# Kernel optimization log

Measured on AMD Instinct MI355X. Metric: run time of the kernel, lower is better.

The kernel has to match this reference:

```python
import jax, jax.numpy as jnp
import numpy as np
from jax import lax

EPS = 1e-5

def _instance_norm(x):
    # per-sample, per-channel over HW, affine=False (torch default), biased var
    m = jnp.mean(x, axis=(2, 3), keepdims=True)
    v = jnp.mean((x - m) ** 2, axis=(2, 3), keepdims=True)
    return (x - m) / jnp.sqrt(v + EPS)

def _lrelu(x):
    return jax.nn.leaky_relu(x, 0.2)

def _conv(x, w, b, stride=1, pad=0):
    y = lax.conv_general_dilated(x, w, (stride, stride), ((pad, pad), (pad, pad)),
                                 dimension_numbers=('NCHW', 'OIHW', 'NCHW'))
    return y + b[None, :, None, None]

def _conv_transpose(x, w, b):
    # torch ConvTranspose2d(k=3, stride=2, padding=1, output_padding=1)
    # == dilated conv with lhs_dilation=2, pad (k-1-p, k-1-p+op) = (1, 2),
    # kernel spatially flipped and in/out swapped. w: (Cin, Cout, 3, 3)
    wt = jnp.flip(w, axis=(2, 3)).transpose(1, 0, 2, 3)  # (Cout, Cin, 3, 3)
    y = lax.conv_general_dilated(x, wt, (1, 1), ((1, 2), (1, 2)),
                                 lhs_dilation=(2, 2),
                                 dimension_numbers=('NCHW', 'OIHW', 'NCHW'))
    return y + b[None, :, None, None]

def _reflect_pad1(x):
    return jnp.pad(x, ((0, 0), (0, 0), (1, 1), (1, 1)), mode='reflect')

def _nearest_resize(x, out_h, out_w):
    in_h, in_w = x.shape[2], x.shape[3]
    iy = (jnp.arange(out_h) * (in_h / out_h)).astype(jnp.int32)
    ix = (jnp.arange(out_w) * (in_w / out_w)).astype(jnp.int32)
    return x[:, :, iy][:, :, :, ix]

def setup_inputs() -> dict:
    key = jax.random.key(0)
    ks = jax.random.split(key, 12)
    B, S, H, W = 8, 19, 256, 256
    out_nc = 512
    inp = jax.random.normal(ks[0], (B, 3, H, W), dtype=jnp.float32)
    labels = jax.random.randint(ks[1], (B, 1, H, W), 0, S)
    segmap = (labels == jnp.arange(S).reshape(1, S, 1, 1)).astype(jnp.float32)
    sc = 0.05
    return {
        'input': inp, 'segmap': segmap,
        'w1': jax.random.normal(ks[2], (32, 3, 3, 3), jnp.float32) * sc,
        'b1': jnp.zeros((32,), jnp.float32),
        'w2': jax.random.normal(ks[3], (64, 32, 3, 3), jnp.float32) * sc,
        'b2': jnp.zeros((64,), jnp.float32),
        'w3': jax.random.normal(ks[4], (128, 64, 3, 3), jnp.float32) * sc,
        'b3': jnp.zeros((128,), jnp.float32),
        'w4': jax.random.normal(ks[5], (128, 256, 3, 3), jnp.float32) * sc,  # torch convT layout (Cin, Cout, kh, kw)
        'b4': jnp.zeros((256,), jnp.float32),
        'w5': jax.random.normal(ks[6], (out_nc, 256, 3, 3), jnp.float32) * sc,
        'b5': jnp.zeros((out_nc,), jnp.float32),
    }

def _backbone(x, w1, b1, w2, b2, w3, b3, w4, b4, w5, b5):
    x = _lrelu(_instance_norm(_conv(_reflect_pad1(x), w1, b1)))          # [B,32,256,256]
    x = _lrelu(_instance_norm(_conv(x, w2, b2, stride=2, pad=1)))        # [B,64,128,128]
    x = _lrelu(_instance_norm(_conv(x, w3, b3, stride=2, pad=1)))        # [B,128,64,64]
    x = _lrelu(_instance_norm(_conv_transpose(x, w4, b4)))               # [B,256,128,128]
    x = jnp.tanh(_conv(_reflect_pad1(x), w5, b5))                        # [B,512,128,128]
    return x

def reference(input, segmap, w1, b1, w2, b2, w3, b3, w4, b4, w5, b5):
    codes = _backbone(input, w1, b1, w2, b2, w3, b3, w4, b4, w5, b5)
    seg = _nearest_resize(segmap, codes.shape[2], codes.shape[3])
    mask = (seg > 0).astype(codes.dtype)                                  # segmap.bool()
    sums = jnp.einsum('bchw,bshw->bsc', codes, mask)                      # masked sum per (b, class)
    counts = jnp.sum(mask, axis=(2, 3))[:, :, None]                       # [B,S,1]
    return jnp.where(counts > 0, sums / jnp.maximum(counts, 1.0), 0.0)    # [B,S,C]
```

## Files before the change

kernel.cpp:

```cpp
#include <hip/hip_runtime.h>

#define LB __launch_bounds__(256)

constexpr int S = 19;

typedef __attribute__((ext_vector_type(8))) short frag16;
typedef __attribute__((ext_vector_type(8))) ushort ushort8;
typedef __attribute__((ext_vector_type(4))) float f32x4;

__device__ __forceinline__ int reflect256(int i) { return i < 0 ? -i : (i > 255 ? 510 - i : i); }
__device__ __forceinline__ int reflect128(int i) { return i < 0 ? -i : (i > 127 ? 254 - i : i); }

__device__ __forceinline__ ushort f2bf(float f) {
    union { float f; uint u; } a; a.f = f;
    uint r = a.u + 0x7fffu + ((a.u >> 16) & 1u);
    return (ushort)(r >> 16);
}
__device__ __forceinline__ float bf2f(ushort u) {
    union { uint u; float f; } a; a.u = ((uint)u) << 16; return a.f;
}

__device__ __forceinline__ void gll16(const void* g, void* l) {
    __builtin_amdgcn_global_load_lds(
        (const __attribute__((address_space(1))) void*)g,
        (__attribute__((address_space(3))) void*)l, 16, 0, 0);
}

__global__ LB void k_conv1cl(const float* __restrict__ in, const float* __restrict__ w,
                             const float* __restrict__ bias, ushort* __restrict__ out) {
    __shared__ float Wr[864];
    __shared__ float Bs[32];
    int t = threadIdx.x;
    for (int e = t; e < 864; e += 256) Wr[e] = w[e];
    if (t < 32) Bs[t] = bias[t];
    __syncthreads();
    int idx = blockIdx.x * 256 + t;
    int x = idx & 255, y = (idx >> 8) & 255, b = idx >> 16;
    float v[27];
    #pragma unroll
    for (int ci = 0; ci < 3; ++ci) {
        const float* ip = in + ((b * 3 + ci) << 16);
        #pragma unroll
        for (int ky = 0; ky < 3; ++ky) {
            int iy = reflect256(y + ky - 1);
            #pragma unroll
            for (int kx = 0; kx < 3; ++kx) {
                int ix = reflect256(x + kx - 1);
                v[ci * 9 + ky * 3 + kx] = ip[(iy << 8) + ix];
            }
        }
    }
    ushort* op = out + (long)idx * 32;
    #pragma unroll
    for (int g = 0; g < 4; ++g) {
        ushort8 o;
        #pragma unroll
        for (int j = 0; j < 8; ++j) {
            int co = g * 8 + j;
            float a = Bs[co];
            #pragma unroll
            for (int k = 0; k < 27; ++k) a += v[k] * Wr[co * 27 + k];
            o[j] = f2bf(a);
        }
        *(ushort8*)(op + g * 8) = o;
    }
}

template <int C, int PB, int SPLITS>
__global__ LB void k_stats_cl(const ushort* __restrict__ x,
                              float* __restrict__ psum, float* __restrict__ pss) {
    __shared__ float lsum[C], lss[C];
    int b = blockIdx.x / SPLITS, sp = blockIdx.x % SPLITS;
    int t = threadIdx.x;
    if (t < C) { lsum[t] = 0.f; lss[t] = 0.f; }
    __syncthreads();
    constexpr int CG = C / 8;
    constexpr int PO = 256 / CG;
    int c0 = (t % CG) * 8;
    int po = t / CG;
    float s[8], ss[8];
    #pragma unroll
    for (int k = 0; k < 8; ++k) { s[k] = 0.f; ss[k] = 0.f; }
    const ushort* base = x + ((long)b * SPLITS + sp) * (long)PB * C;
    for (int p = po; p < PB; p += PO) {
        ushort8 v = *(const ushort8*)(base + (long)p * C + c0);
        #pragma unroll
        for (int k = 0; k < 8; ++k) {
            float f = bf2f(v[k]);
            s[k] += f; ss[k] += f * f;
        }
    }
    #pragma unroll
    for (int k = 0; k < 8; ++k) {
        atomicAdd(&lsum[c0 + k], s[k]);
        atomicAdd(&lss[c0 + k], ss[k]);
    }
    __syncthreads();
    if (t < C) {
        psum[blockIdx.x * C + t] = lsum[t];
        pss[blockIdx.x * C + t] = lss[t];
    }
}

template <int C, int SPLITS, int P>
__global__ LB void k_red_cl(const float* __restrict__ psum, const float* __restrict__ pss,
                            float* __restrict__ mean, float* __restrict__ istd) {
    int idx = blockIdx.x * 256 + threadIdx.x;
    if (idx >= 8 * C) return;
    int b = idx / C, c = idx % C;
    float s = 0.f, ss = 0.f;
    for (int sp = 0; sp < SPLITS; ++sp) {
        s += psum[(b * SPLITS + sp) * C + c];
        ss += pss[(b * SPLITS + sp) * C + c];
    }
    float m = s / (float)P;
    float v = ss / (float)P - m * m;
    mean[idx] = m;
    istd[idx] = rsqrtf(v + 1e-5f);
}

template <int C, int P>
__global__ LB void k_nl_cl(ushort* __restrict__ x, const float* __restrict__ mean,
                           const float* __restrict__ istd) {
    long e = ((long)blockIdx.x * 256 + threadIdx.x) * 8;
    int c0 = (int)(e % C);
    int b = (int)(e / ((long)P * C));
    ushort8 v = *(ushort8*)(x + e);
    const float* mp = mean + b * C + c0;
    const float* ip = istd + b * C + c0;
    #pragma unroll
    for (int k = 0; k < 8; ++k) {
        float u = (bf2f(v[k]) - mp[k]) * ip[k];
        u = u > 0.f ? u : 0.2f * u;
        v[k] = f2bf(u);
    }
    *(ushort8*)(x + e) = v;
}

__global__ LB void k_wtall(const float* __restrict__ w2, const float* __restrict__ w3,
                           const float* __restrict__ w4, const float* __restrict__ w5,
                           ushort* __restrict__ t2, ushort* __restrict__ t3,
                           ushort* __restrict__ t4, ushort* __restrict__ t5) {
    int e = blockIdx.x * 256 + threadIdx.x;
    if (e < 18432) {
        int ci = e & 31, co = (e >> 5) & 63, tap = e >> 11;
        t2[e] = f2bf(w2[(co * 32 + ci) * 9 + tap]);
    } else if (e < 18432 + 73728) {
        int e2 = e - 18432;
        int ci = e2 & 63, co = (e2 >> 6) & 127, tap = e2 >> 13;
        t3[e2] = f2bf(w3[(co * 64 + ci) * 9 + tap]);
    } else if (e < 18432 + 73728 + 294912) {
        int e3 = e - (18432 + 73728);
        int ci = e3 & 127, co = (e3 >> 7) & 255, tap = e3 >> 15;
        t4[e3] = f2bf(w4[ci * 2304 + co * 9 + tap]);
    } else {
        int e4 = e - (18432 + 73728 + 294912);
        int ci = e4 & 255, co = (e4 >> 8) & 511, tap = e4 >> 17;
        t5[e4] = f2bf(w5[(co * 256 + ci) * 9 + tap]);
    }
}

__global__ LB void k_conv2m(const ushort* __restrict__ xin, const ushort* __restrict__ wt,
                            const float* __restrict__ bias, ushort* __restrict__ xout) {
    int bx = blockIdx.x;
    int y = bx & 127, b = bx >> 7;
    int t = threadIdx.x, w = t >> 6, lane = t & 63;
    int col0 = w * 32;
    int lanep = lane & 15, hi = lane >> 4;

    f32x4 acc[4][2];
    #pragma unroll
    for (int m = 0; m < 4; ++m)
        #pragma unroll
        for (int n = 0; n < 2; ++n) acc[m][n] = (f32x4){0.f, 0.f, 0.f, 0.f};

    #pragma unroll
    for (int ky = 0; ky < 3; ++ky) {
        int iy = 2 * y + ky - 1;
        if (iy < 0) continue;
        #pragma unroll
        for (int kx = 0; kx < 3; ++kx) {
            int tap = ky * 3 + kx;
            const ushort* wb = wt + ((tap * 64 + lanep) << 5) + hi * 8;
            frag16 av[4];
            #pragma unroll
            for (int m = 0; m < 4; ++m) av[m] = *(const frag16*)(wb + ((m * 16) << 5));
            frag16 bv[2];
            #pragma unroll
            for (int n = 0; n < 2; ++n) {
                int xo = col0 + n * 16 + lanep;
                int ix = 2 * xo + kx - 1;
                frag16 vv = (frag16)(short)0;
                if (ix >= 0)
                    vv = *(const frag16*)(xin + ((((long)(b * 256 + iy)) << 8) + ix) * 32 + hi * 8);
                bv[n] = vv;
            }
            #pragma unroll
            for (int m = 0; m < 4; ++m)
                #pragma unroll
                for (int n = 0; n < 2; ++n)
                    acc[m][n] = __builtin_amdgcn_mfma_f32_16x16x32_bf16(av[m], bv[n], acc[m][n], 0, 0, 0);
        }
    }
    float bvv[4][4];
    #pragma unroll
    for (int m = 0; m < 4; ++m)
        #pragma unroll
        for (int r = 0; r < 4; ++r) bvv[m][r] = bias[m * 16 + hi * 4 + r];
    #pragma unroll
    for (int n = 0; n < 2; ++n) {
        int xo = col0 + n * 16 + lanep;
        long pb = ((((long)(b * 128 + y)) << 7) + xo) * 64 + hi * 4;
        #pragma unroll
        for (int m = 0; m < 4; ++m) {
            ushort4 o;
            o.x = f2bf(acc[m][n][0] + bvv[m][0]);
            o.y = f2bf(acc[m][n][1] + bvv[m][1]);
            o.z = f2bf(acc[m][n][2] + bvv[m][2]);
            o.w = f2bf(acc[m][n][3] + bvv[m][3]);
            *(ushort4*)(xout + pb + m * 16) = o;
        }
    }
}

__global__ LB void k_conv3m(const ushort* __restrict__ xin, const ushort* __restrict__ wt,
                            const float* __restrict__ bias, ushort* __restrict__ xout) {
    int bx = blockIdx.x;
    int y = bx & 63, b = bx >> 6;
    int t = threadIdx.x, w = t >> 6, lane = t & 63;
    int co0 = (w >> 1) * 64;
    int col0 = (w & 1) * 32;
    int lanep = lane & 15, hi = lane >> 4;

    f32x4 acc[4][2];
    #pragma unroll
    for (int m = 0; m < 4; ++m)
        #pragma unroll
        for (int n = 0; n < 2; ++n) acc[m][n] = (f32x4){0.f, 0.f, 0.f, 0.f};

    #pragma unroll
    for (int ky = 0; ky < 3; ++ky) {
        int iy = 2 * y + ky - 1;
        if (iy < 0) continue;
        #pragma unroll
        for (int kx = 0; kx < 3; ++kx) {
            int tap = ky * 3 + kx;
            #pragma unroll
            for (int ck = 0; ck < 2; ++ck) {
                int ci0 = ck * 32;
                const ushort* wb = wt + ((tap * 128 + co0 + lanep) << 6) + ci0 + hi * 8;
                frag16 av[4];
                #pragma unroll
                for (int m = 0; m < 4; ++m) av[m] = *(const frag16*)(wb + ((m * 16) << 6));
                frag16 bv[2];
                #pragma unroll
                for (int n = 0; n < 2; ++n) {
                    int xo = col0 + n * 16 + lanep;
                    int ix = 2 * xo + kx - 1;
                    frag16 vv = (frag16)(short)0;
                    if (ix >= 0)
                        vv = *(const frag16*)(xin + ((((long)(b * 128 + iy)) << 7) + ix) * 64 + ci0 + hi * 8);
                    bv[n] = vv;
                }
                #pragma unroll
                for (int m = 0; m < 4; ++m)
                    #pragma unroll
                    for (int n = 0; n < 2; ++n)
                        acc[m][n] = __builtin_amdgcn_mfma_f32_16x16x32_bf16(av[m], bv[n], acc[m][n], 0, 0, 0);
            }
        }
    }
    float bvv[4][4];
    #pragma unroll
    for (int m = 0; m < 4; ++m)
        #pragma unroll
        for (int r = 0; r < 4; ++r) bvv[m][r] = bias[co0 + m * 16 + hi * 4 + r];
    #pragma unroll
    for (int n = 0; n < 2; ++n) {
        int xo = col0 + n * 16 + lanep;
        long pb = ((((long)(b * 64 + y)) << 6) + xo) * 128 + co0 + hi * 4;
        #pragma unroll
        for (int m = 0; m < 4; ++m) {
            ushort4 o;
            o.x = f2bf(acc[m][n][0] + bvv[m][0]);
            o.y = f2bf(acc[m][n][1] + bvv[m][1]);
            o.z = f2bf(acc[m][n][2] + bvv[m][2]);
            o.w = f2bf(acc[m][n][3] + bvv[m][3]);
            *(ushort4*)(xout + pb + m * 16) = o;
        }
    }
}

__global__ LB void k_convt4m(const ushort* __restrict__ x3l, const ushort* __restrict__ wt,
                             const float* __restrict__ bias, ushort* __restrict__ xl) {
    int bx = blockIdx.x;
    int parity = bx & 3;
    int py = parity >> 1, px = parity & 1;
    int rg = (bx >> 2) & 15;
    int ct = (bx >> 6) & 3;
    int b  = bx >> 8;
    int co0 = ct * 64;
    int t = threadIdx.x;
    int w = t >> 6;
    int ip = rg * 4 + w;
    int lane = t & 63;
    int lanep = lane & 15;
    int hi = lane >> 4;
    int laneq = hi * 8;

    f32x4 acc[4][4];
    #pragma unroll
    for (int m = 0; m < 4; ++m)
        #pragma unroll
        for (int n = 0; n < 4; ++n) acc[m][n] = (f32x4){0.f, 0.f, 0.f, 0.f};

    #pragma unroll
    for (int ky = 0; ky < 3; ++ky) {
        if (((ky + py) & 1) == 0) continue;
        int i = ip + ((py == 1 && ky == 0) ? 1 : 0);
        if (i >= 64) continue;
        #pragma unroll
        for (int kx = 0; kx < 3; ++kx) {
            if (((kx + px) & 1) == 0) continue;
            int dxp = (px == 1 && kx == 0) ? 1 : 0;
            int tap = ky * 3 + kx;
            const ushort* wbase = wt + (((long)tap * 256 + co0 + lanep) << 7) + laneq;
            const ushort* xbase = x3l + ((((long)b << 12) + (i << 6)) << 7) + laneq;
            #pragma unroll
            for (int ci0 = 0; ci0 < 128; ci0 += 32) {
                frag16 av[4], bv[4];
                #pragma unroll
                for (int m = 0; m < 4; ++m)
                    av[m] = *(const frag16*)(wbase + ((m * 16) << 7) + ci0);
                #pragma unroll
                for (int n = 0; n < 4; ++n) {
                    int j = n * 16 + lanep + dxp;
                    bool valid = j < 64;
                    frag16 v = *(const frag16*)(xbase + ((valid ? j : 63) << 7) + ci0);
                    if (!valid) v = (frag16)(short)0;
                    bv[n] = v;
                }
                #pragma unroll
                for (int m = 0; m < 4; ++m)
                    #pragma unroll
                    for (int n = 0; n < 4; ++n)
                        acc[m][n] = __builtin_amdgcn_mfma_f32_16x16x32_bf16(av[m], bv[n], acc[m][n], 0, 0, 0);
            }
        }
    }

    float bvv[4][4];
    #pragma unroll
    for (int m = 0; m < 4; ++m)
        #pragma unroll
        for (int r = 0; r < 4; ++r)
            bvv[m][r] = bias[co0 + m * 16 + hi * 4 + r];
    int y = 2 * ip + py;
    #pragma unroll
    for (int n = 0; n < 4; ++n) {
        int x = 2 * (n * 16 + lanep) + px;
        long pb = ((((long)b << 14) + (y << 7) + x) << 8) + co0 + hi * 4;
        #pragma unroll
        for (int m = 0; m < 4; ++m) {
            ushort4 o;
            o.x = f2bf(acc[m][n][0] + bvv[m][0]);
            o.y = f2bf(acc[m][n][1] + bvv[m][1]);
            o.z = f2bf(acc[m][n][2] + bvv[m][2]);
            o.w = f2bf(acc[m][n][3] + bvv[m][3]);
            *(ushort4*)(xl + pb + m * 16) = o;
        }
    }
}

__global__ LB void k_label(const float* __restrict__ segmap, int* __restrict__ lab,
                           int* __restrict__ counts) {
    __shared__ int h[S];
    if (threadIdx.x < S) h[threadIdx.x] = 0;
    __syncthreads();
    int idx = blockIdx.x * 256 + threadIdx.x;
    int x = idx & 127, y = (idx >> 7) & 127, b = idx >> 14;
    const float* sp = segmap + (long)b * S * 65536 + (y << 1) * 256 + (x << 1);
    int s = 0;
    for (int c = 0; c < S; ++c) {
        if (sp[c * 65536] > 0.f) { s = c; break; }
    }
    lab[idx] = s;
    atomicAdd(&h[s], 1);
    __syncthreads();
    if (threadIdx.x < S) atomicAdd(&counts[b * S + threadIdx.x], h[threadIdx.x]);
}

__global__ void __launch_bounds__(512, 1)
k_conv5m(const ushort* __restrict__ xl, const ushort* __restrict__ wt,
         const float* __restrict__ bias, const int* __restrict__ lab,
         float* __restrict__ sumbuf) {
    __shared__ __align__(16) ushort L[57856];
    float* part = (float*)L;
    constexpr int XS0 = 0, XS1 = 16640, WS0 = 33280, WS1 = 45568;

    int bx = blockIdx.x;
    int yp = bx & 63;
    int ct = (bx >> 6) & 3;
    int b  = bx >> 8;
    int y0 = yp * 2, cob = ct * 128;
    int t = threadIdx.x;
    int w = t >> 6;
    int lane = t & 63;
    int row_w = w & 1;
    int col0 = ((w >> 1) & 1) * 64;
    int coh = w >> 2;
    int cobw = cob + coh * 64;
    int lanep = lane & 15;
    int hi = lane >> 4;
    int wkey8 = (hi ^ ((lanep >> 1) & 3)) * 8;

    long xbase = (long)b << 14;
    long xg[4]; long xgt = 0;
    #pragma unroll
    for (int k = 0; k < 4; ++k) {
        int e = t + k * 512;
        int q = e & 3, p = e >> 2;
        int qp = q ^ ((p >> 1) & 3);
        int r = p / 130, c = p - r * 130;
        int gy = reflect128(y0 - 1 + r);
        int gc = reflect128(c - 1);
        xg[k] = ((xbase + (gy << 7) + gc) << 8) + qp * 8;
    }
    if (t < 32) {
        int e = 2048 + t;
        int q = e & 3, p = e >> 2;
        int qp = q ^ ((p >> 1) & 3);
        int r = p / 130, c = p - r * 130;
        int gy = reflect128(y0 - 1 + r);
        int gc = reflect128(c - 1);
        xgt = ((xbase + (gy << 7) + gc) << 8) + qp * 8;
    }
    int wgb[3];
    #pragma unroll
    for (int k = 0; k < 3; ++k) {
        int f = t + k * 512;
        int q = f & 3, p = f >> 2;
        int qp = q ^ ((p >> 1) & 3);
        int tapin = p >> 7, co = p & 127;
        wgb[k] = ((tapin * 512 + cob + co) << 8) + qp * 8;
    }

    f32x4 acc[4][4];
    #pragma unroll
    for (int m = 0; m < 4; ++m)
        #pragma unroll
        for (int n = 0; n < 4; ++n) acc[m][n] = (f32x4){0.f, 0.f, 0.f, 0.f};

    #define ISSUE_X(c) {                                                              \
        int cin = (c) * 32; int xd = ((c) & 1) ? XS1 : XS0;                           \
        _Pragma("unroll")                                                             \
        for (int k = 0; k < 4; ++k) gll16(xl + xg[k] + cin, L + xd + (t + k * 512) * 8); \
        if (t < 32) gll16(xl + xgt + cin, L + xd + (2048 + t) * 8); }

    #define ISSUE_W(c, g) {                                                           \
        int cin = (c) * 32; int wd = ((3 * (c) + (g)) & 1) ? WS1 : WS0;               \
        _Pragma("unroll")                                                             \
        for (int k = 0; k < 3; ++k)                                                   \
            gll16(wt + wgb[k] + (g) * 393216 + cin, L + wd + (t + k * 512) * 8); }

    #define SYNC_PRE() { __builtin_amdgcn_sched_barrier(0);                           \
        __builtin_amdgcn_s_barrier(); __builtin_amdgcn_sched_barrier(0); }
    #define SYNC_POST() { __builtin_amdgcn_sched_barrier(0); __builtin_amdgcn_s_barrier(); }

    #define COMPUTE(c, g) {                                                           \
        const ushort* xs  = L + (((c) & 1) ? XS1 : XS0);                              \
        const ushort* wsb = L + (((3 * (c) + (g)) & 1) ? WS1 : WS0);                  \
        _Pragma("unroll")                                                             \
        for (int tapin = 0; tapin < 3; ++tapin) {                                     \
            frag16 av[4];                                                             \
            _Pragma("unroll")                                                         \
            for (int m = 0; m < 4; ++m)                                               \
                av[m] = *(const frag16*)(wsb + tapin * 4096 + coh * 2048 + m * 512    \
                                         + lanep * 32 + wkey8);                       \
            int p0 = (row_w + (g)) * 130 + col0 + tapin + lanep;                      \
            int bo = p0 * 32 + (hi ^ ((p0 >> 1) & 3)) * 8;                            \
            frag16 bf[4];                                                             \
            _Pragma("unroll")                                                         \
            for (int n = 0; n < 4; ++n) bf[n] = *(const frag16*)(xs + bo + n * 512);  \
            _Pragma("unroll")                                                         \
            for (int m = 0; m < 4; ++m)                                               \
                _Pragma("unroll")                                                     \
                for (int n = 0; n < 4; ++n)                                           \
                    acc[m][n] = __builtin_amdgcn_mfma_f32_16x16x32_bf16(av[m], bf[n], acc[m][n], 0, 0, 0); \
        } }

    ISSUE_X(0);
    ISSUE_W(0, 0);
    asm volatile("s_waitcnt vmcnt(0)" ::: "memory");
    SYNC_PRE();

    #pragma unroll 1
    for (int c = 0; c < 8; ++c) {
        if (c < 7) { ISSUE_X(c + 1); }
        ISSUE_W(c, 1);
        if (c < 7) { asm volatile("s_waitcnt vmcnt(7)" ::: "memory"); }
        else       { asm volatile("s_waitcnt vmcnt(3)" ::: "memory"); }
        SYNC_PRE();
        COMPUTE(c, 0);
        SYNC_POST();
        ISSUE_W(c, 2);
        asm volatile("s_waitcnt vmcnt(3)" ::: "memory");
        SYNC_PRE();
        COMPUTE(c, 1);
        SYNC_POST();
        if (c < 7) {
            ISSUE_W(c + 1, 0);
            asm volatile("s_waitcnt vmcnt(3)" ::: "memory");
        } else {
            asm volatile("s_waitcnt vmcnt(0)" ::: "memory");
        }
        SYNC_PRE();
        COMPUTE(c, 2);
        SYNC_POST();
    }
    #undef ISSUE_X
    #undef ISSUE_W
    #undef COMPUTE
    #undef SYNC_PRE
    #undef SYNC_POST

    float bv[4][4];
    #pragma unroll
    for (int m = 0; m < 4; ++m)
        #pragma unroll
        for (int r = 0; r < 4; ++r)
            bv[m][r] = bias[cobw + m * 16 + hi * 4 + r];

    for (int e = t; e < S * 128; e += 512) part[e] = 0.f;
    __syncthreads();

    int y = y0 + row_w;
    int colc = coh * 64;
    #pragma unroll
    for (int n = 0; n < 4; ++n) {
        int x = col0 + n * 16 + lanep;
        int s = lab[(b << 14) + (y << 7) + x];
        #pragma unroll
        for (int m = 0; m < 4; ++m)
            #pragma unroll
            for (int r = 0; r < 4; ++r)
                atomicAdd(&part[s * 128 + colc + m * 16 + hi * 4 + r], tanhf(acc[m][n][r] + bv[m][r]));
    }
    __syncthreads();
    for (int e = t; e < S * 128; e += 512) {
        int s = e >> 7, cc = e & 127;
        atomicAdd(&sumbuf[((b * S + s) << 9) + cob + cc], part[e]);
    }
}

__global__ LB void k_final(const float* __restrict__ sumbuf, const int* __restrict__ counts,
                           float* __restrict__ out) {
    int idx = blockIdx.x * 256 + threadIdx.x;
    int tt = idx >> 9;
    int s = tt % S, b = tt / S;
    int cnt = counts[b * S + s];
    out[idx] = cnt > 0 ? sumbuf[idx] / (float)cnt : 0.f;
}

extern "C" void kernel_launch(void* const* d_in, const int* in_sizes, int n_in,
                              void* d_out, int out_size, void* d_ws, size_t ws_size,
                              hipStream_t stream) {
    const float* input  = (const float*)d_in[0];
    const float* segmap = (const float*)d_in[1];
    const float* w1 = (const float*)d_in[2];  const float* b1 = (const float*)d_in[3];
    const float* w2 = (const float*)d_in[4];  const float* b2 = (const float*)d_in[5];
    const float* w3 = (const float*)d_in[6];  const float* b3 = (const float*)d_in[7];
    const float* w4 = (const float*)d_in[8];  const float* b4 = (const float*)d_in[9];
    const float* w5 = (const float*)d_in[10]; const float* b5 = (const float*)d_in[11];
    float* out = (float*)d_out;

    float* ws = (float*)d_ws;
    ushort* xl    = (ushort*)ws;
    ushort* x1l   = (ushort*)(ws + 16777216);
    ushort* x2l   = (ushort*)(ws + 25165824);
    ushort* x3l   = (ushort*)(ws + 29360128);
    float* sumbuf = ws + 31457280;
    float* mean   = ws + 31535104;
    float* istd   = ws + 31537152;
    int*   lab    = (int*)(ws + 31539200);
    int*   counts = (int*)(ws + 31670272);
    ushort* wt5   = (ushort*)(ws + 31670528);
    ushort* wt4t  = (ushort*)(ws + 32260352);
    ushort* wt2   = (ushort*)(ws + 32407808);
    ushort* wt3   = (ushort*)(ws + 32417024);
    float* psum   = ws + 32453888;
    float* pss    = ws + 32519424;

    hipMemsetAsync(sumbuf, 0, 77824 * sizeof(float), stream);
    hipMemsetAsync(counts, 0, 256 * sizeof(int), stream);

    k_wtall<<<6120, 256, 0, stream>>>(w2, w3, w4, w5, wt2, wt3, wt4t, wt5);
    k_conv1cl<<<2048, 256, 0, stream>>>(input, w1, b1, x1l);
    k_stats_cl<32, 1024, 64><<<512, 256, 0, stream>>>(x1l, psum, pss);
    k_red_cl<32, 64, 65536><<<1, 256, 0, stream>>>(psum, pss, mean, istd);
    k_nl_cl<32, 65536><<<8192, 256, 0, stream>>>(x1l, mean, istd);
    k_conv2m<<<1024, 256, 0, stream>>>(x1l, wt2, b2, x2l);
    k_stats_cl<64, 512, 32><<<256, 256, 0, stream>>>(x2l, psum, pss);
    k_red_cl<64, 32, 16384><<<2, 256, 0, stream>>>(psum, pss, mean, istd);
    k_nl_cl<64, 16384><<<4096, 256, 0, stream>>>(x2l, mean, istd);
    k_conv3m<<<512, 256, 0, stream>>>(x2l, wt3, b3, x3l);
    k_stats_cl<128, 256, 16><<<128, 256, 0, stream>>>(x3l, psum, pss);
    k_red_cl<128, 16, 4096><<<4, 256, 0, stream>>>(psum, pss, mean, istd);
    k_nl_cl<128, 4096><<<2048, 256, 0, stream>>>(x3l, mean, istd);
    k_convt4m<<<2048, 256, 0, stream>>>(x3l, wt4t, b4, xl);
    k_stats_cl<256, 512, 32><<<256, 256, 0, stream>>>(xl, psum, pss);
    k_red_cl<256, 32, 16384><<<8, 256, 0, stream>>>(psum, pss, mean, istd);
    k_nl_cl<256, 16384><<<16384, 256, 0, stream>>>(xl, mean, istd);
    k_label<<<512, 256, 0, stream>>>(segmap, lab, counts);
    k_conv5m<<<2048, 512, 0, stream>>>(xl, wt5, b5, lab, sumbuf);
    k_final<<<304, 256, 0, stream>>>(sumbuf, counts, out);
}
```

Measured before the change: 938.0 us.

## Fuse instance-norm statistics into conv epilogues and raise MFMA priority in conv5

```diff
diff --git a/kernel.cpp b/kernel.cpp
--- a/kernel.cpp
+++ b/kernel.cpp
@@ -160,8 +160,15 @@
     }
 }
 
+__device__ __forceinline__ void statred(float s, float q, int lane, float* ps, float* qs) {
+    s += __shfl_xor(s, 1); s += __shfl_xor(s, 2); s += __shfl_xor(s, 4); s += __shfl_xor(s, 8);
+    q += __shfl_xor(q, 1); q += __shfl_xor(q, 2); q += __shfl_xor(q, 4); q += __shfl_xor(q, 8);
+    if ((lane & 15) == 0) { atomicAdd(ps, s); atomicAdd(qs, q); }
+}
+
 __global__ LB void k_conv2m(const ushort* __restrict__ xin, const ushort* __restrict__ wt,
-                            const float* __restrict__ bias, ushort* __restrict__ xout) {
+                            const float* __restrict__ bias, ushort* __restrict__ xout,
+                            float* __restrict__ psum, float* __restrict__ pss) {
     int bx = blockIdx.x;
     int y = bx & 127, b = bx >> 7;
     int t = threadIdx.x, w = t >> 6, lane = t & 63;
@@ -202,11 +209,14 @@
                     acc[m][n] = __builtin_amdgcn_mfma_f32_16x16x32_bf16(av[m], bv[n], acc[m][n], 0, 0, 0);
         }
     }
-    float bvv[4][4];
-    #pragma unroll
-    for (int m = 0; m < 4; ++m)
-        #pragma unroll
-        for (int r = 0; r < 4; ++r) bvv[m][r] = bias[m * 16 + hi * 4 + r];
+    float bvv[4][4], s16[4][4], q16[4][4];
+    #pragma unroll
+    for (int m = 0; m < 4; ++m)
+        #pragma unroll
+        for (int r = 0; r < 4; ++r) {
+            bvv[m][r] = bias[m * 16 + hi * 4 + r];
+            s16[m][r] = 0.f; q16[m][r] = 0.f;
+        }
     #pragma unroll
     for (int n = 0; n < 2; ++n) {
         int xo = col0 + n * 16 + lanep;
@@ -214,17 +224,28 @@
         #pragma unroll
         for (int m = 0; m < 4; ++m) {
             ushort4 o;
-            o.x = f2bf(acc[m][n][0] + bvv[m][0]);
-            o.y = f2bf(acc[m][n][1] + bvv[m][1]);
-            o.z = f2bf(acc[m][n][2] + bvv[m][2]);
-            o.w = f2bf(acc[m][n][3] + bvv[m][3]);
+            float vv[4];
+            #pragma unroll
+            for (int r = 0; r < 4; ++r) {
+                vv[r] = acc[m][n][r] + bvv[m][r];
+                s16[m][r] += vv[r]; q16[m][r] += vv[r] * vv[r];
+            }
+            o.x = f2bf(vv[0]); o.y = f2bf(vv[1]); o.z = f2bf(vv[2]); o.w = f2bf(vv[3]);
             *(ushort4*)(xout + pb + m * 16) = o;
         }
     }
+    #pragma unroll
+    for (int m = 0; m < 4; ++m)
+        #pragma unroll
+        for (int r = 0; r < 4; ++r) {
+            int c = m * 16 + hi * 4 + r;
+            statred(s16[m][r], q16[m][r], lane, &psum[b * 64 + c], &pss[b * 64 + c]);
+        }
 }
 
 __global__ LB void k_conv3m(const ushort* __restrict__ xin, const ushort* __restrict__ wt,
-                            const float* __restrict__ bias, ushort* __restrict__ xout) {
+                            const float* __restrict__ bias, ushort* __restrict__ xout,
+                            float* __restrict__ psum, float* __restrict__ pss) {
     int bx = blockIdx.x;
     int y = bx & 63, b = bx >> 6;
     int t = threadIdx.x, w = t >> 6, lane = t & 63;
@@ -270,11 +291,14 @@
             }
         }
     }
-    float bvv[4][4];
-    #pragma unroll
-    for (int m = 0; m < 4; ++m)
-        #pragma unroll
-        for (int r = 0; r < 4; ++r) bvv[m][r] = bias[co0 + m * 16 + hi * 4 + r];
+    float bvv[4][4], s16[4][4], q16[4][4];
+    #pragma unroll
+    for (int m = 0; m < 4; ++m)
+        #pragma unroll
+        for (int r = 0; r < 4; ++r) {
+            bvv[m][r] = bias[co0 + m * 16 + hi * 4 + r];
+            s16[m][r] = 0.f; q16[m][r] = 0.f;
+        }
     #pragma unroll
     for (int n = 0; n < 2; ++n) {
         int xo = col0 + n * 16 + lanep;
@@ -282,17 +306,28 @@
         #pragma unroll
         for (int m = 0; m < 4; ++m) {
             ushort4 o;
-            o.x = f2bf(acc[m][n][0] + bvv[m][0]);
-            o.y = f2bf(acc[m][n][1] + bvv[m][1]);
-            o.z = f2bf(acc[m][n][2] + bvv[m][2]);
-            o.w = f2bf(acc[m][n][3] + bvv[m][3]);
+            float vv[4];
+            #pragma unroll
+            for (int r = 0; r < 4; ++r) {
+                vv[r] = acc[m][n][r] + bvv[m][r];
+                s16[m][r] += vv[r]; q16[m][r] += vv[r] * vv[r];
+            }
+            o.x = f2bf(vv[0]); o.y = f2bf(vv[1]); o.z = f2bf(vv[2]); o.w = f2bf(vv[3]);
             *(ushort4*)(xout + pb + m * 16) = o;
         }
     }
+    #pragma unroll
+    for (int m = 0; m < 4; ++m)
+        #pragma unroll
+        for (int r = 0; r < 4; ++r) {
+            int c = co0 + m * 16 + hi * 4 + r;
+            statred(s16[m][r], q16[m][r], lane, &psum[b * 128 + c], &pss[b * 128 + c]);
+        }
 }
 
 __global__ LB void k_convt4m(const ushort* __restrict__ x3l, const ushort* __restrict__ wt,
-                             const float* __restrict__ bias, ushort* __restrict__ xl) {
+                             const float* __restrict__ bias, ushort* __restrict__ xl,
+                             float* __restrict__ psum, float* __restrict__ pss) {
     int bx = blockIdx.x;
     int parity = bx & 3;
     int py = parity >> 1, px = parity & 1;
@@ -349,12 +384,14 @@
         }
     }
 
-    float bvv[4][4];
-    #pragma unroll
-    for (int m = 0; m < 4; ++m)
-        #pragma unroll
-        for (int r = 0; r < 4; ++r)
+    float bvv[4][4], s16[4][4], q16[4][4];
+    #pragma unroll
+    for (int m = 0; m < 4; ++m)
+        #pragma unroll
+        for (int r = 0; r < 4; ++r) {
             bvv[m][r] = bias[co0 + m * 16 + hi * 4 + r];
+            s16[m][r] = 0.f; q16[m][r] = 0.f;
+        }
     int y = 2 * ip + py;
     #pragma unroll
     for (int n = 0; n < 4; ++n) {
@@ -363,13 +400,23 @@
         #pragma unroll
         for (int m = 0; m < 4; ++m) {
             ushort4 o;
-            o.x = f2bf(acc[m][n][0] + bvv[m][0]);
-            o.y = f2bf(acc[m][n][1] + bvv[m][1]);
-            o.z = f2bf(acc[m][n][2] + bvv[m][2]);
-            o.w = f2bf(acc[m][n][3] + bvv[m][3]);
+            float vv[4];
+            #pragma unroll
+            for (int r = 0; r < 4; ++r) {
+                vv[r] = acc[m][n][r] + bvv[m][r];
+                s16[m][r] += vv[r]; q16[m][r] += vv[r] * vv[r];
+            }
+            o.x = f2bf(vv[0]); o.y = f2bf(vv[1]); o.z = f2bf(vv[2]); o.w = f2bf(vv[3]);
             *(ushort4*)(xl + pb + m * 16) = o;
         }
     }
+    #pragma unroll
+    for (int m = 0; m < 4; ++m)
+        #pragma unroll
+        for (int r = 0; r < 4; ++r) {
+            int c = co0 + m * 16 + hi * 4 + r;
+            statred(s16[m][r], q16[m][r], lane, &psum[b * 256 + c], &pss[b * 256 + c]);
+        }
 }
 
 __global__ LB void k_label(const float* __restrict__ segmap, int* __restrict__ lab,
@@ -482,11 +529,13 @@
             frag16 bf[4];                                                             \
             _Pragma("unroll")                                                         \
             for (int n = 0; n < 4; ++n) bf[n] = *(const frag16*)(xs + bo + n * 512);  \
+            __builtin_amdgcn_s_setprio(1);                                            \
             _Pragma("unroll")                                                         \
             for (int m = 0; m < 4; ++m)                                               \
                 _Pragma("unroll")                                                     \
                 for (int n = 0; n < 4; ++n)                                           \
                     acc[m][n] = __builtin_amdgcn_mfma_f32_16x16x32_bf16(av[m], bf[n], acc[m][n], 0, 0, 0); \
+            __builtin_amdgcn_s_setprio(0);                                            \
         } }
 
     ISSUE_X(0);
@@ -590,26 +639,30 @@
     ushort* wt3   = (ushort*)(ws + 32417024);
     float* psum   = ws + 32453888;
     float* pss    = ws + 32519424;
+    float* psum2  = ws + 32584960;
+    float* pss2   = ws + 32585472;
+    float* psum3  = ws + 32585984;
+    float* pss3   = ws + 32587008;
+    float* psum4  = ws + 32588032;
+    float* pss4   = ws + 32590080;
 
     hipMemsetAsync(sumbuf, 0, 77824 * sizeof(float), stream);
     hipMemsetAsync(counts, 0, 256 * sizeof(int), stream);
+    hipMemsetAsync(psum2, 0, 7168 * sizeof(float), stream);
 
     k_wtall<<<6120, 256, 0, stream>>>(w2, w3, w4, w5, wt2, wt3, wt4t, wt5);
     k_conv1cl<<<2048, 256, 0, stream>>>(input, w1, b1, x1l);
     k_stats_cl<32, 1024, 64><<<512, 256, 0, stream>>>(x1l, psum, pss);
     k_red_cl<32, 64, 65536><<<1, 256, 0, stream>>>(psum, pss, mean, istd);
     k_nl_cl<32, 65536><<<8192, 256, 0, stream>>>(x1l, mean, istd);
-    k_conv2m<<<1024, 256, 0, stream>>>(x1l, wt2, b2, x2l);
-    k_stats_cl<64, 512, 32><<<256, 256, 0, stream>>>(x2l, psum, pss);
-    k_red_cl<64, 32, 16384><<<2, 256, 0, stream>>>(psum, pss, mean, istd);
+    k_conv2m<<<1024, 256, 0, stream>>>(x1l, wt2, b2, x2l, psum2, pss2);
+    k_red_cl<64, 1, 16384><<<2, 256, 0, stream>>>(psum2, pss2, mean, istd);
     k_nl_cl<64, 16384><<<4096, 256, 0, stream>>>(x2l, mean, istd);
-    k_conv3m<<<512, 256, 0, stream>>>(x2l, wt3, b3, x3l);
-    k_stats_cl<128, 256, 16><<<128, 256, 0, stream>>>(x3l, psum, pss);
-    k_red_cl<128, 16, 4096><<<4, 256, 0, stream>>>(psum, pss, mean, istd);
+    k_conv3m<<<512, 256, 0, stream>>>(x2l, wt3, b3, x3l, psum3, pss3);
+    k_red_cl<128, 1, 4096><<<4, 256, 0, stream>>>(psum3, pss3, mean, istd);
     k_nl_cl<128, 4096><<<2048, 256, 0, stream>>>(x3l, mean, istd);
-    k_convt4m<<<2048, 256, 0, stream>>>(x3l, wt4t, b4, xl);
-    k_stats_cl<256, 512, 32><<<256, 256, 0, stream>>>(xl, psum, pss);
-    k_red_cl<256, 32, 16384><<<8, 256, 0, stream>>>(psum, pss, mean, istd);
+    k_convt4m<<<2048, 256, 0, stream>>>(x3l, wt4t, b4, xl, psum4, pss4);
+    k_red_cl<256, 1, 16384><<<8, 256, 0, stream>>>(psum4, pss4, mean, istd);
     k_nl_cl<256, 16384><<<16384, 256, 0, stream>>>(xl, mean, istd);
     k_label<<<512, 256, 0, stream>>>(segmap, lab, counts);
     k_conv5m<<<2048, 512, 0, stream>>>(xl, wt5, b5, lab, sumbuf);
```

Measured after the change: 1.024 ms. 1.09x slower.
